# Performance work log

Hardware: AMD Instinct MI355X
Metric: run time of the kernel (lower is better)

The kernel has to match this reference:

```python
import jax, jax.numpy as jnp
import numpy as np

N_Q = 50000
BATCH = 512
SEQLEN = 500
MEM_SIZE = 64
DK = 128   # key_embedding_dim == key_memory_state_dim == final_fc_dim
DV = 256   # value_embedding_dim == value_memory_state_dim
FC = 128


def setup_inputs() -> dict:
    key = jax.random.key(0)
    ks = jax.random.split(key, 16)
    q_data = jax.random.randint(ks[0], (BATCH, SEQLEN), 0, N_Q + 1, dtype=jnp.int64)
    qa_data = jax.random.randint(ks[1], (BATCH, SEQLEN), 0, 2 * N_Q + 1, dtype=jnp.int64)
    u = jax.random.uniform(ks[2], (BATCH * SEQLEN, 1))
    target = jnp.where(u < 0.1, -1.0, jnp.round(jax.random.uniform(ks[3], (BATCH * SEQLEN, 1)))).astype(jnp.float32)
    # embedding tables with padding_idx=0 zeroed
    q_embed_W = (jax.random.normal(ks[4], (N_Q + 1, DK)) * (2.0 / DK) ** 0.5).at[0].set(0.0)
    qa_embed_W = (jax.random.normal(ks[5], (2 * N_Q + 1, DV)) * (2.0 / DV) ** 0.5).at[0].set(0.0)
    key_memory = jax.random.normal(ks[6], (MEM_SIZE, DK)) * (2.0 / DK) ** 0.5
    init_value_memory = jax.random.normal(ks[7], (MEM_SIZE, DV)) * (2.0 / DV) ** 0.5
    erase_W = jax.random.normal(ks[8], (DV, DV)) * (2.0 / DV) ** 0.5
    erase_b = jnp.zeros((DV,))
    add_W = jax.random.normal(ks[9], (DV, DV)) * (2.0 / DV) ** 0.5
    add_b = jnp.zeros((DV,))
    read_W = jax.random.normal(ks[10], (FC, DV + DK)) * (2.0 / (DV + DK)) ** 0.5
    read_b = jnp.zeros((FC,))
    pred_W = jax.random.normal(ks[11], (1, FC)) * (2.0 / FC) ** 0.5
    pred_b = jnp.zeros((1,))
    return dict(q_data=q_data, qa_data=qa_data, target=target,
                q_embed_W=q_embed_W, qa_embed_W=qa_embed_W,
                key_memory=key_memory, init_value_memory=init_value_memory,
                erase_W=erase_W, erase_b=erase_b, add_W=add_W, add_b=add_b,
                read_W=read_W, read_b=read_b, pred_W=pred_W, pred_b=pred_b)


def reference(q_data, qa_data, target, q_embed_W, qa_embed_W, key_memory,
              init_value_memory, erase_W, erase_b, add_W, add_b,
              read_W, read_b, pred_W, pred_b):
    B, S = q_data.shape
    q_e = q_embed_W[q_data]    # (B, S, DK)
    qa_e = qa_embed_W[qa_data]  # (B, S, DV)

    # Addressing weights do not depend on the value memory state -> batch them.
    cw = jax.nn.softmax(jnp.einsum('bsk,mk->bsm', q_e, key_memory), axis=-1)  # (B,S,M)
    erase = jax.nn.sigmoid(jnp.einsum('bsv,ev->bse', qa_e, erase_W) + erase_b)  # (B,S,DV)
    add = jnp.tanh(jnp.einsum('bsv,ev->bse', qa_e, add_W) + add_b)              # (B,S,DV)

    def step(mem, xs):
        w, er, ad = xs  # (B,M), (B,DV), (B,DV)
        read = jnp.einsum('bm,bmd->bd', w, mem)  # read before write
        mem = mem * (1.0 - w[:, :, None] * er[:, None, :]) + w[:, :, None] * ad[:, None, :]
        return mem, read

    init_mem = jnp.broadcast_to(init_value_memory, (B,) + init_value_memory.shape)
    _, reads = jax.lax.scan(step, init_mem,
                            (jnp.swapaxes(cw, 0, 1), jnp.swapaxes(erase, 0, 1), jnp.swapaxes(add, 0, 1)))
    reads = jnp.swapaxes(reads, 0, 1)  # (B, S, DV)

    predict_input = jnp.concatenate([reads, q_e], axis=-1).reshape(B * S, -1)
    h = jnp.tanh(predict_input @ read_W.T + read_b)
    logits = h @ pred_W.T + pred_b  # (B*S, 1)

    mask = target >= 0.0
    # numerically-stable BCE with logits
    bce = jnp.maximum(logits, 0.0) - logits * target + jnp.log1p(jnp.exp(-jnp.abs(logits)))
    denom = jnp.maximum(jnp.sum(mask.astype(logits.dtype)), 1.0)
    loss = jnp.sum(jnp.where(mask, bce, 0.0)) / denom
    # masked_select replaced by masked full-size outputs for static shapes
    pred_masked = jnp.where(mask, jax.nn.sigmoid(logits), 0.0)
    target_masked = jnp.where(mask, target, 0.0)
    return loss, pred_masked, target_masked
```

## Files before the change

kernel.cpp:

```cpp
#include <hip/hip_runtime.h>
#include <hip/hip_bf16.h>

#define BATCH 512
#define SEQ   500
#define BS    (BATCH*SEQ)
#define MEM   64
#define DK    128
#define DV    256
#define FC    128
#define KS    16

typedef float f32x4 __attribute__((ext_vector_type(4)));
typedef unsigned int u32x4 __attribute__((ext_vector_type(4)));
typedef unsigned int u32x2 __attribute__((ext_vector_type(2)));
typedef unsigned short u16x8 __attribute__((ext_vector_type(8)));
typedef __bf16 bf16x8 __attribute__((ext_vector_type(8)));

__device__ __forceinline__ float bf2f(unsigned short u){ return __uint_as_float(((unsigned)u)<<16); }
__device__ __forceinline__ unsigned short f2bfu(float x){
  unsigned u = __float_as_uint(x);
  return (unsigned short)((u + 0x7FFFu + ((u>>16)&1u)) >> 16);
}
__device__ __forceinline__ float sigf(float x){ return 1.f/(1.f+__expf(-x)); }
__device__ __forceinline__ float tanh_fast(float x){ return 2.f/(1.f+__expf(-2.f*x)) - 1.f; }

#define DPP_ADD(r, ctrl) { \
  int _s = __builtin_amdgcn_update_dpp(0, __builtin_bit_cast(int, r), ctrl, 0xF, 0xF, true); \
  r += __builtin_bit_cast(float, _s); \
}

__device__ __forceinline__ float ldF(const void* p, long i, int f32m){
  return f32m ? ((const float*)p)[i] : bf2f(((const unsigned short*)p)[i]);
}
__device__ __forceinline__ int ldI(const int* p, long i, int i64m){
  return i64m ? p[2*i] : p[i];
}
__device__ __forceinline__ void st8(unsigned short* dst, const void* src, long i, int f32m){
  if (f32m){
    const float* q = (const float*)src + i;
    f32x4 a = *(const f32x4*)q;
    f32x4 b = *(const f32x4*)(q+4);
    u16x8 o;
    o[0]=f2bfu(a[0]); o[1]=f2bfu(a[1]); o[2]=f2bfu(a[2]); o[3]=f2bfu(a[3]);
    o[4]=f2bfu(b[0]); o[5]=f2bfu(b[1]); o[6]=f2bfu(b[2]); o[7]=f2bfu(b[3]);
    *(u16x8*)dst = o;
  } else {
    *(u16x8*)dst = *(const u16x8*)((const unsigned short*)src + i);
  }
}
__device__ __forceinline__ void stOut(void* p, long i, float x, int f32m){
  if (f32m) ((float*)p)[i] = x;
  else ((unsigned short*)p)[i] = f2bfu(x);
}

__global__ void k_detect(const unsigned short* __restrict__ km, const int* __restrict__ qa,
                         int* __restrict__ flags, float* __restrict__ accum){
  int t = threadIdx.x;
  if (t < 2) accum[t] = 0.f;
  unsigned short u = km[2*t];
  int e = (u >> 7) & 0xFF;
  bool sane = (e==0) || (e>=100 && e<=140);
  unsigned long long sm = __ballot(sane);
  unsigned long long zm = __ballot(qa[2*t+1] == 0);
  if (t == 0){
    flags[0] = (__popcll(sm) < 48) ? 1 : 0;
    flags[1] = (zm == 0xFFFFFFFFFFFFFFFFull) ? 1 : 0;
  }
}

__global__ __launch_bounds__(256, 2) void k_cw(const int* __restrict__ qd,
    const void* __restrict__ qW, const void* __restrict__ keym,
    float* __restrict__ cw, const int* __restrict__ flags){
  const int f32m = flags[0], i64m = flags[1];
  __shared__ float keyT[DK][MEM];
  int t = threadIdx.x;
  for (int i=t;i<MEM*DK;i+=256){ int m=i&63, k=i>>6; keyT[k][m] = ldF(keym, (long)m*DK+k, f32m); }
  __syncthreads();
  long row = (long)blockIdx.x*256 + t;
  int qid = ldI(qd, row, i64m);
  long qb = (long)qid*DK;
  f32x4 A[16];
  #pragma unroll
  for (int g=0;g<16;g++) A[g] = (f32x4){0.f,0.f,0.f,0.f};
  for (int kk=0;kk<DK;kk+=8){
    float qv[8];
    if (f32m){
      const float* qp = (const float*)qW + qb + kk;
      f32x4 a=*(const f32x4*)qp, b=*(const f32x4*)(qp+4);
      qv[0]=a[0];qv[1]=a[1];qv[2]=a[2];qv[3]=a[3];qv[4]=b[0];qv[5]=b[1];qv[6]=b[2];qv[7]=b[3];
    } else {
      u16x8 u = *(const u16x8*)((const unsigned short*)qW + qb + kk);
      #pragma unroll
      for (int j=0;j<8;j++) qv[j]=bf2f(u[j]);
    }
    #pragma unroll
    for (int j=0;j<8;j++){
      float q = qv[j];
      #pragma unroll
      for (int g=0;g<16;g++){
        f32x4 kv = *(const f32x4*)&keyT[kk+j][g*4];
        f32x4 a = A[g];
        a[0]=fmaf(q,kv[0],a[0]); a[1]=fmaf(q,kv[1],a[1]);
        a[2]=fmaf(q,kv[2],a[2]); a[3]=fmaf(q,kv[3],a[3]);
        A[g]=a;
      }
    }
  }
  float mx = -1e30f;
  #pragma unroll
  for (int g=0;g<16;g++){
    f32x4 a = A[g];
    mx = fmaxf(mx, fmaxf(fmaxf(a[0],a[1]), fmaxf(a[2],a[3])));
  }
  float sum = 0.f;
  #pragma unroll
  for (int g=0;g<16;g++){
    f32x4 a = A[g];
    a[0]=__expf(a[0]-mx); a[1]=__expf(a[1]-mx); a[2]=__expf(a[2]-mx); a[3]=__expf(a[3]-mx);
    sum += (a[0]+a[1])+(a[2]+a[3]);
    A[g]=a;
  }
  float inv = 1.f/sum;
  float* outp = cw + row*MEM;
  #pragma unroll
  for (int g=0;g<16;g++){
    f32x4 a = A[g];
    f32x4 v = { a[0]*inv, a[1]*inv, a[2]*inv, a[3]*inv };
    *(f32x4*)(outp + g*4) = v;
  }
}

__global__ __launch_bounds__(256, 2) void k_ea(const int* __restrict__ qad, long row0,
    const void* __restrict__ qaW, const void* __restrict__ eW, const void* __restrict__ ebias,
    const void* __restrict__ aW, const void* __restrict__ abias,
    unsigned short* __restrict__ ea, const int* __restrict__ flags, int nwg){
  const int f32m = flags[0], i64m = flags[1];
  __shared__ unsigned short As[128][40];
  __shared__ unsigned short Bs[128][40];
  __shared__ int rid[128];
  int g = blockIdx.x;
  int x = g & 7, idx = g >> 3;
  int qq = nwg >> 3, rr = nwg & 7;
  int base = (x < rr) ? x*(qq+1) : rr*(qq+1) + (x-rr)*qq;
  int orig = base + idx;
  int bm = orig >> 2, bn = orig & 3;

  int t = threadIdx.x;
  if (t < 128) rid[t] = ldI(qad, row0 + (long)bm*128 + t, i64m);
  int lane = t & 63, wid = t >> 6;
  int wr = wid >> 1, wc = wid & 1;
  f32x4 acc[4][4] = {};
  for (int k0=0;k0<DV;k0+=32){
    __syncthreads();
    #pragma unroll
    for (int j=0;j<2;j++){
      int c = t*2+j, r = c>>2, ko = (c&3)*8;
      st8(&As[r][ko], qaW, (long)rid[r]*DV + k0 + ko, f32m);
      if (r < 64) st8(&Bs[r][ko], eW, (long)(64*bn + r)*DV + k0 + ko, f32m);
      else        st8(&Bs[r][ko], aW, (long)(64*bn + r - 64)*DV + k0 + ko, f32m);
    }
    __syncthreads();
    bf16x8 af[4], bfr[4];
    #pragma unroll
    for (int i=0;i<4;i++){
      af[i]  = __builtin_bit_cast(bf16x8, *(const u16x8*)&As[wr*64+i*16+(lane&15)][(lane>>4)*8]);
      bfr[i] = __builtin_bit_cast(bf16x8, *(const u16x8*)&Bs[wc*64+i*16+(lane&15)][(lane>>4)*8]);
    }
    #pragma unroll
    for (int i=0;i<4;i++)
      #pragma unroll
      for (int n=0;n<4;n++)
        acc[i][n] = __builtin_amdgcn_mfma_f32_16x16x32_bf16(af[i], bfr[n], acc[i][n],0,0,0);
  }
  #pragma unroll
  for (int i=0;i<4;i++)
    #pragma unroll
    for (int n=0;n<4;n++){
      int cc = n*16 + (lane&15);
      int gcol = 64*bn + cc;
      float bias = wc ? ldF(abias,gcol,f32m) : ldF(ebias,gcol,f32m);
      int dcol = 2*gcol + wc;
      #pragma unroll
      for (int rix=0;rix<4;rix++){
        long rowg = (long)bm*128 + wr*64 + i*16 + (lane>>4)*4 + rix;
        float v = acc[i][n][rix] + bias;
        float o = wc ? tanh_fast(v) : sigf(v);
        ea[rowg*(2*DV) + dcol] = f2bfu(o);
      }
    }
}

#define SCAN_STEP2(srel) { \
  f32x4 W0 = *(const f32x4*)(wb + (srel)*MEM); \
  f32x4 W1 = *(const f32x4*)(wb + (srel)*MEM + 4); \
  u32x2 uu = *(const u32x2*)(eb + (srel)*256); \
  float er0 = __uint_as_float(uu[0] << 16); \
  float ad0 = __uint_as_float(uu[0] & 0xFFFF0000u); \
  float er1 = __uint_as_float(uu[1] << 16); \
  float ad1 = __uint_as_float(uu[1] & 0xFFFF0000u); \
  float ra0=0.f, ra1=0.f, rb0=0.f, rb1=0.f; \
  _Pragma("unroll") \
  for (int j=0; j<8; j++){ \
    float w = (j<4) ? W0[j] : W1[j-4]; \
    if (j & 1) ra1 = fmaf(w, MA[j], ra1); else ra0 = fmaf(w, MA[j], ra0); \
    float ta = fmaf(MA[j], er0, -ad0); \
    MA[j] = fmaf(-w, ta, MA[j]); \
    if (j & 1) rb1 = fmaf(w, MB[j], rb1); else rb0 = fmaf(w, MB[j], rb0); \
    float tb = fmaf(MB[j], er1, -ad1); \
    MB[j] = fmaf(-w, tb, MB[j]); \
  } \
  float r0 = ra0 + ra1; \
  float r1 = rb0 + rb1; \
  DPP_ADD(r0, 0x111); DPP_ADD(r0, 0x112); DPP_ADD(r0, 0x114); \
  DPP_ADD(r1, 0x111); DPP_ADD(r1, 0x112); DPP_ADD(r1, 0x114); \
  if (q == 7){ \
    unsigned pk; \
    asm("v_cvt_pk_bf16_f32 %0, %1, %2" : "=v"(pk) : "v"(r0), "v"(r1)); \
    rdu[(srel)*128] = pk; \
  } \
}

__global__ __launch_bounds__(1024, 4) void k_scan(const float* __restrict__ cw,
    const unsigned short* __restrict__ ea, const void* __restrict__ initm,
    unsigned short* __restrict__ rdout, const int* __restrict__ flags){
  const int f32m = flags[0];
  __shared__ float        w_lds[2][KS][MEM];
  __shared__ unsigned int ea_lds[2][KS][DV];
  int b = blockIdx.x;
  int t = threadIdx.x;
  int q = t & 7;
  int dp = t >> 3;
  int d0 = 2*dp;
  int m0 = q * 8;

  float MA[8], MB[8];
  #pragma unroll
  for (int g=0; g<8; g++){
    MA[g] = ldF(initm, (long)(m0+g)*DV + d0,   f32m);
    MB[g] = ldF(initm, (long)(m0+g)*DV + d0+1, f32m);
  }

  const float* cwb = cw + (long)b*SEQ*MEM;
  const unsigned int* epb = (const unsigned int*)(ea + (long)b*SEQ*(2*DV));
  unsigned int* rdu = (unsigned int*)(rdout + (long)b*SEQ*DV) + dp;

  {
    float wreg = cwb[t];
    u32x4 ereg = *(const u32x4*)(epb + t*4);
    ((float*)w_lds[0])[t] = wreg;
    *(u32x4*)((unsigned int*)ea_lds[0] + t*4) = ereg;
  }
  __syncthreads();

  int cur = 0;
  for (int st = 0; st < 31; st++){
    float wnext = cwb[(st+1)*KS*MEM + t];
    u32x4 enext = *(const u32x4*)(epb + (st+1)*KS*DV + t*4);

    const float* wb        = (const float*)w_lds[cur] + m0;
    const unsigned int* eb = (const unsigned int*)ea_lds[cur] + d0;
    #pragma unroll
    for (int srel=0; srel<KS; srel++){
      SCAN_STEP2(srel);
    }
    ((float*)w_lds[cur^1])[t] = wnext;
    *(u32x4*)((unsigned int*)ea_lds[cur^1] + t*4) = enext;
    rdu += KS*128;
    __syncthreads();
    cur ^= 1;
  }
  {
    const float* wb        = (const float*)w_lds[cur] + m0;
    const unsigned int* eb = (const unsigned int*)ea_lds[cur] + d0;
    #pragma unroll
    for (int srel=0; srel<4; srel++){
      SCAN_STEP2(srel);
    }
  }
}

__global__ __launch_bounds__(256, 2) void k_pred(const int* __restrict__ qd, long row0,
    const void* __restrict__ qW, const unsigned short* __restrict__ rds,
    const void* __restrict__ rW, const void* __restrict__ rb,
    const void* __restrict__ pW, const void* __restrict__ pb,
    const void* __restrict__ target,
    void* __restrict__ out, float* __restrict__ accum,
    const int* __restrict__ flags){
  const int f32m = flags[0], i64m = flags[1];
  __shared__ unsigned short As[128][40];
  __shared__ unsigned short Bs[128][40];
  __shared__ unsigned short hs[128][136];
  __shared__ int rid[128];
  int t = threadIdx.x;
  int bm = blockIdx.x;
  if (t<128) rid[t] = ldI(qd, row0 + (long)bm*128+t, i64m);
  int lane=t&63, wid=t>>6, wr=wid>>1, wc=wid&1;
  f32x4 acc[4][4] = {};
  for (int k0=0;k0<(DV+DK);k0+=32){
    __syncthreads();
    #pragma unroll
    for (int j=0;j<2;j++){
      int c=t*2+j, r=c>>2, ko=(c&3)*8;
      if (k0 < DV) st8(&As[r][ko], rds, ((long)bm*128+r)*DV + k0+ko, 0);
      else         st8(&As[r][ko], qW, (long)rid[r]*DK + (k0-DV)+ko, f32m);
      st8(&Bs[r][ko], rW, (long)r*(DV+DK) + k0+ko, f32m);
    }
    __syncthreads();
    bf16x8 af[4], bfr[4];
    #pragma unroll
    for (int i=0;i<4;i++){
      af[i]  = __builtin_bit_cast(bf16x8, *(const u16x8*)&As[wr*64+i*16+(lane&15)][(lane>>4)*8]);
      bfr[i] = __builtin_bit_cast(bf16x8, *(const u16x8*)&Bs[wc*64+i*16+(lane&15)][(lane>>4)*8]);
    }
    #pragma unroll
    for (int i=0;i<4;i++)
      #pragma unroll
      for (int n=0;n<4;n++)
        acc[i][n] = __builtin_amdgcn_mfma_f32_16x16x32_bf16(af[i], bfr[n], acc[i][n],0,0,0);
  }
  #pragma unroll
  for (int i=0;i<4;i++)
    #pragma unroll
    for (int n=0;n<4;n++){
      int col = wc*64 + n*16 + (lane&15);
      float bias = ldF(rb, col, f32m);
      #pragma unroll
      for (int rix=0;rix<4;rix++){
        int rowl = wr*64 + i*16 + (lane>>4)*4 + rix;
        hs[rowl][col] = f2bfu(tanh_fast(acc[i][n][rix] + bias));
      }
    }
  __syncthreads();
  float bces = 0.f, cnts = 0.f;
  if (t < 128){
    float lg = ldF(pb, 0, f32m);
    #pragma unroll
    for (int cc=0;cc<FC;cc++) lg = fmaf(bf2f(hs[t][cc]), ldF(pW, cc, f32m), lg);
    long rowg = row0 + (long)bm*128 + t;
    float tg = ldF(target, rowg, f32m);
    bool mask = tg >= 0.f;
    float e = __expf(-fabsf(lg));
    float bce = fmaxf(lg, 0.f) - lg*tg + __logf(1.f + e);
    bces = mask ? bce : 0.f;
    cnts = mask ? 1.f : 0.f;
    stOut(out, 1 + rowg, mask ? sigf(lg) : 0.f, f32m);
    stOut(out, 1 + BS + rowg, mask ? tg : 0.f, f32m);
  }
  #pragma unroll
  for (int off=32; off>0; off>>=1){ bces += __shfl_down(bces, off); cnts += __shfl_down(cnts, off); }
  if ((t & 63) == 0 && t < 128){
    atomicAdd(&accum[0], bces);
    atomicAdd(&accum[1], cnts);
  }
}

__global__ void k_loss(const float* __restrict__ accum, void* __restrict__ out,
                       const int* __restrict__ flags){
  if (threadIdx.x == 0){
    float denom = fmaxf(accum[1], 1.f);
    stOut(out, 0, accum[0]/denom, flags[0]);
  }
}

extern "C" void kernel_launch(void* const* d_in, const int* in_sizes, int n_in,
                              void* d_out, int out_size, void* d_ws, size_t ws_size,
                              hipStream_t stream) {
  const int* q_data  = (const int*)d_in[0];
  const int* qa_data = (const int*)d_in[1];
  const void* target = d_in[2];
  const void* qW   = d_in[3];
  const void* qaW  = d_in[4];
  const void* keym = d_in[5];
  const void* initm= d_in[6];
  const void* eW   = d_in[7];
  const void* eb   = d_in[8];
  const void* aW   = d_in[9];
  const void* ab   = d_in[10];
  const void* rW   = d_in[11];
  const void* rb   = d_in[12];
  const void* pW   = d_in[13];
  const void* pb   = d_in[14];

  char* ws = (char*)d_ws;
  const size_t CW_OFF = 256;
  const size_t CW_BYTES = (size_t)BS*MEM*4;
  const size_t EA_OFF = CW_OFF + CW_BYTES;
  float* accum = (float*)ws;
  int* flags = (int*)(ws + 64);
  float* cw = (float*)(ws + CW_OFF);

  const long per_batch = (long)SEQ*(2*DV)*2 + (long)SEQ*DV*2;
  long rem = (long)ws_size - (long)EA_OFF;
  int bchunk = 512;
  while (bchunk > 32 && per_batch*bchunk > rem) bchunk >>= 1;

  const size_t EA_BYTES = (size_t)bchunk*SEQ*(2*DV)*2;
  unsigned short* ea = (unsigned short*)(ws + EA_OFF);
  unsigned short* rd = (unsigned short*)(ws + EA_OFF + EA_BYTES);

  k_detect<<<1, 64, 0, stream>>>((const unsigned short*)keym, qa_data, flags, accum);
  k_cw  <<<BS/256, 256, 0, stream>>>(q_data, qW, keym, cw, flags);

  int nchunk = BATCH / bchunk;
  for (int c = 0; c < nchunk; c++){
    long b0 = (long)c * bchunk;
    int rows = bchunk * SEQ;
    int nwg = (rows/128)*4;
    k_ea  <<<nwg, 256, 0, stream>>>(qa_data, b0*SEQ, qaW, eW, eb, aW, ab, ea, flags, nwg);
    k_scan<<<bchunk, 1024, 0, stream>>>(cw + b0*SEQ*MEM, ea, initm, rd, flags);
    k_pred<<<rows/128, 256, 0, stream>>>(q_data, b0*SEQ, qW, rd, rW, rb, pW, pb,
                                         target, d_out, accum, flags);
  }
  k_loss<<<1, 64, 0, stream>>>(accum, d_out, flags);
}
```

Measured before the change: 984.6 us.

## Split scan across two blocks per batch along value dim; raise occupancy elsewhere

The scan kernel now launches two 512-thread blocks per batch element, each owning half of the value dimension, so each block stages only half of the erase/add tile in LDS and more, smaller blocks can be scheduled. The DPP reduction is rewritten as inline v_add_f32_dpp instructions, which removes the separate update_dpp moves. k_ea and k_pred raise their min-blocks launch bound to 3, and k_pred aliases its GEMM staging buffers with the hidden-state buffer (adding a barrier) to cut LDS use. The cw weight tile is now loaded redundantly by both halves, and the tighter launch bounds may cause register spills.

After: 1.040 ms. 1.06x slower.

```diff
diff --git a/kernel.cpp b/kernel.cpp
--- a/kernel.cpp
+++ b/kernel.cpp
@@ -11,6 +11,7 @@
 #define KS    16
 
 typedef float f32x4 __attribute__((ext_vector_type(4)));
+typedef float f32x2 __attribute__((ext_vector_type(2)));
 typedef unsigned int u32x4 __attribute__((ext_vector_type(4)));
 typedef unsigned int u32x2 __attribute__((ext_vector_type(2)));
 typedef unsigned short u16x8 __attribute__((ext_vector_type(8)));
@@ -24,9 +25,10 @@
 __device__ __forceinline__ float sigf(float x){ return 1.f/(1.f+__expf(-x)); }
 __device__ __forceinline__ float tanh_fast(float x){ return 2.f/(1.f+__expf(-2.f*x)) - 1.f; }
 
-#define DPP_ADD(r, ctrl) { \
-  int _s = __builtin_amdgcn_update_dpp(0, __builtin_bit_cast(int, r), ctrl, 0xF, 0xF, true); \
-  r += __builtin_bit_cast(float, _s); \
+#define DPP3(r) { \
+  asm("v_add_f32_dpp %0, %0, %0 row_shr:1 row_mask:0xf bank_mask:0xf bound_ctrl:0" : "+v"(r)); \
+  asm("v_add_f32_dpp %0, %0, %0 row_shr:2 row_mask:0xf bank_mask:0xf bound_ctrl:0" : "+v"(r)); \
+  asm("v_add_f32_dpp %0, %0, %0 row_shr:4 row_mask:0xf bank_mask:0xf bound_ctrl:0" : "+v"(r)); \
 }
 
 __device__ __forceinline__ float ldF(const void* p, long i, int f32m){
@@ -130,7 +132,7 @@
   }
 }
 
-__global__ __launch_bounds__(256, 2) void k_ea(const int* __restrict__ qad, long row0,
+__global__ __launch_bounds__(256, 3) void k_ea(const int* __restrict__ qad, long row0,
     const void* __restrict__ qaW, const void* __restrict__ eW, const void* __restrict__ ebias,
     const void* __restrict__ aW, const void* __restrict__ abias,
     unsigned short* __restrict__ ea, const int* __restrict__ flags, int nwg){
@@ -193,7 +195,7 @@
 #define SCAN_STEP2(srel) { \
   f32x4 W0 = *(const f32x4*)(wb + (srel)*MEM); \
   f32x4 W1 = *(const f32x4*)(wb + (srel)*MEM + 4); \
-  u32x2 uu = *(const u32x2*)(eb + (srel)*256); \
+  u32x2 uu = *(const u32x2*)(eb + (srel)*128); \
   float er0 = __uint_as_float(uu[0] << 16); \
   float ad0 = __uint_as_float(uu[0] & 0xFFFF0000u); \
   float er1 = __uint_as_float(uu[1] << 16); \
@@ -211,8 +213,8 @@
   } \
   float r0 = ra0 + ra1; \
   float r1 = rb0 + rb1; \
-  DPP_ADD(r0, 0x111); DPP_ADD(r0, 0x112); DPP_ADD(r0, 0x114); \
-  DPP_ADD(r1, 0x111); DPP_ADD(r1, 0x112); DPP_ADD(r1, 0x114); \
+  DPP3(r0); \
+  DPP3(r1); \
   if (q == 7){ \
     unsigned pk; \
     asm("v_cvt_pk_bf16_f32 %0, %1, %2" : "=v"(pk) : "v"(r0), "v"(r1)); \
@@ -220,17 +222,17 @@
   } \
 }
 
-__global__ __launch_bounds__(1024, 4) void k_scan(const float* __restrict__ cw,
+__global__ __launch_bounds__(512, 4) void k_scan(const float* __restrict__ cw,
     const unsigned short* __restrict__ ea, const void* __restrict__ initm,
     unsigned short* __restrict__ rdout, const int* __restrict__ flags){
   const int f32m = flags[0];
   __shared__ float        w_lds[2][KS][MEM];
-  __shared__ unsigned int ea_lds[2][KS][DV];
-  int b = blockIdx.x;
+  __shared__ unsigned int ea_lds[2][KS][128];
+  int b = blockIdx.x, y = blockIdx.y;
   int t = threadIdx.x;
   int q = t & 7;
   int dp = t >> 3;
-  int d0 = 2*dp;
+  int d0 = y*128 + 2*dp;
   int m0 = q * 8;
 
   float MA[8], MB[8];
@@ -241,37 +243,37 @@
   }
 
   const float* cwb = cw + (long)b*SEQ*MEM;
-  const unsigned int* epb = (const unsigned int*)(ea + (long)b*SEQ*(2*DV));
-  unsigned int* rdu = (unsigned int*)(rdout + (long)b*SEQ*DV) + dp;
+  const unsigned int* epb = (const unsigned int*)(ea + (long)b*SEQ*(2*DV)) + y*128;
+  unsigned int* rdu = (unsigned int*)(rdout + (long)b*SEQ*DV) + y*64 + dp;
 
   {
-    float wreg = cwb[t];
-    u32x4 ereg = *(const u32x4*)(epb + t*4);
-    ((float*)w_lds[0])[t] = wreg;
-    *(u32x4*)((unsigned int*)ea_lds[0] + t*4) = ereg;
+    f32x2 wreg = *(const f32x2*)(cwb + 2*t);
+    u32x4 ereg = *(const u32x4*)(epb + (t>>5)*256 + 4*(t&31));
+    ((f32x2*)(&w_lds[0][0][0]))[t] = wreg;
+    ((u32x4*)(&ea_lds[0][0][0]))[t] = ereg;
   }
   __syncthreads();
 
   int cur = 0;
   for (int st = 0; st < 31; st++){
-    float wnext = cwb[(st+1)*KS*MEM + t];
-    u32x4 enext = *(const u32x4*)(epb + (st+1)*KS*DV + t*4);
-
-    const float* wb        = (const float*)w_lds[cur] + m0;
-    const unsigned int* eb = (const unsigned int*)ea_lds[cur] + d0;
+    f32x2 wnext = *(const f32x2*)(cwb + (st+1)*KS*MEM + 2*t);
+    u32x4 enext = *(const u32x4*)(epb + ((st+1)*KS + (t>>5))*256 + 4*(t&31));
+
+    const float* wb        = &w_lds[cur][0][0] + m0;
+    const unsigned int* eb = &ea_lds[cur][0][0] + 2*dp;
     #pragma unroll
     for (int srel=0; srel<KS; srel++){
       SCAN_STEP2(srel);
     }
-    ((float*)w_lds[cur^1])[t] = wnext;
-    *(u32x4*)((unsigned int*)ea_lds[cur^1] + t*4) = enext;
+    ((f32x2*)(&w_lds[cur^1][0][0]))[t] = wnext;
+    ((u32x4*)(&ea_lds[cur^1][0][0]))[t] = enext;
     rdu += KS*128;
     __syncthreads();
     cur ^= 1;
   }
   {
-    const float* wb        = (const float*)w_lds[cur] + m0;
-    const unsigned int* eb = (const unsigned int*)ea_lds[cur] + d0;
+    const float* wb        = &w_lds[cur][0][0] + m0;
+    const unsigned int* eb = &ea_lds[cur][0][0] + 2*dp;
     #pragma unroll
     for (int srel=0; srel<4; srel++){
       SCAN_STEP2(srel);
@@ -279,7 +281,7 @@
   }
 }
 
-__global__ __launch_bounds__(256, 2) void k_pred(const int* __restrict__ qd, long row0,
+__global__ __launch_bounds__(256, 3) void k_pred(const int* __restrict__ qd, long row0,
     const void* __restrict__ qW, const unsigned short* __restrict__ rds,
     const void* __restrict__ rW, const void* __restrict__ rb,
     const void* __restrict__ pW, const void* __restrict__ pb,
@@ -287,10 +289,11 @@
     void* __restrict__ out, float* __restrict__ accum,
     const int* __restrict__ flags){
   const int f32m = flags[0], i64m = flags[1];
-  __shared__ unsigned short As[128][40];
-  __shared__ unsigned short Bs[128][40];
-  __shared__ unsigned short hs[128][136];
+  __shared__ unsigned short pool[128*136];
   __shared__ int rid[128];
+  unsigned short (*As)[40] = (unsigned short (*)[40])pool;
+  unsigned short (*Bs)[40] = (unsigned short (*)[40])(pool + 128*40);
+  unsigned short (*hs)[136] = (unsigned short (*)[136])pool;
   int t = threadIdx.x;
   int bm = blockIdx.x;
   if (t<128) rid[t] = ldI(qd, row0 + (long)bm*128+t, i64m);
@@ -318,6 +321,7 @@
       for (int n=0;n<4;n++)
         acc[i][n] = __builtin_amdgcn_mfma_f32_16x16x32_bf16(af[i], bfr[n], acc[i][n],0,0,0);
   }
+  __syncthreads();
   #pragma unroll
   for (int i=0;i<4;i++)
     #pragma unroll
@@ -407,7 +411,7 @@
     int rows = bchunk * SEQ;
     int nwg = (rows/128)*4;
     k_ea  <<<nwg, 256, 0, stream>>>(qa_data, b0*SEQ, qaW, eW, eb, aW, ab, ea, flags, nwg);
-    k_scan<<<bchunk, 1024, 0, stream>>>(cw + b0*SEQ*MEM, ea, initm, rd, flags);
+    k_scan<<<dim3(bchunk, 2), 512, 0, stream>>>(cw + b0*SEQ*MEM, ea, initm, rd, flags);
     k_pred<<<rows/128, 256, 0, stream>>>(q_data, b0*SEQ, qW, rd, rW, rb, pW, pb,
                                          target, d_out, accum, flags);
   }
```
